# Performance work log

Measured on AMD Instinct MI355X. Metric: run time of the kernel, lower is better.

The kernel has to match this reference:

```python
import jax, jax.numpy as jnp
import numpy as np

NUM_HEADS = 16
WINDOW = 256  # window_size; tokens attend iff |i-j| <= WINDOW//2
LN_EPS = 1e-5


def setup_inputs() -> dict:
    key = jax.random.key(0)
    k1, k2, k3 = jax.random.split(key, 3)
    B, L, D = 2, 2048, 1024
    x = jax.random.normal(k1, (B, L, D), dtype=jnp.float32)
    w_qkv = jax.random.normal(k2, (3 * D, D), dtype=jnp.float32) * 0.02
    w_out = jax.random.normal(k3, (D, D), dtype=jnp.float32) * 0.02
    gamma = jnp.ones((D,), dtype=jnp.float32)
    beta = jnp.zeros((D,), dtype=jnp.float32)
    return {"x": x, "w_qkv": w_qkv, "w_out": w_out, "gamma": gamma, "beta": beta}


def reference(x, w_qkv, w_out, gamma, beta):
    B, L, D = x.shape
    H = NUM_HEADS
    HD = D // H
    residual = x
    # LayerNorm
    mu = jnp.mean(x, axis=-1, keepdims=True)
    var = jnp.mean(jnp.square(x - mu), axis=-1, keepdims=True)
    xn = (x - mu) * jax.lax.rsqrt(var + LN_EPS) * gamma + beta
    # QKV projection (torch Linear: y = x @ W.T)
    qkv = jnp.einsum('bld,ed->ble', xn, w_qkv).reshape(B, L, 3, H, HD)
    qkv = jnp.transpose(qkv, (2, 0, 3, 1, 4))  # [3, B, H, L, HD]
    q, k, v = qkv[0], qkv[1], qkv[2]
    # Dense scores with banded window mask (same math as the torch module)
    scores = jnp.einsum('bhqd,bhkd->bhqk', q, k) / jnp.sqrt(jnp.float32(HD))
    idx = jnp.arange(L)
    band = jnp.abs(idx[:, None] - idx[None, :]) <= (WINDOW // 2)  # [L, L] bool
    scores = jnp.where(band[None, None], scores, -jnp.inf)
    attn = jax.nn.softmax(scores, axis=-1)
    out = jnp.einsum('bhqk,bhkd->bhqd', attn, v)  # [B, H, L, HD]
    out = jnp.transpose(out, (0, 2, 1, 3)).reshape(B, L, D)
    return residual + jnp.einsum('bld,ed->ble', out, w_out)
```

## Files before the change

kernel.cpp:

```cpp
#include <hip/hip_runtime.h>

typedef unsigned int u32;
typedef unsigned short u16;
typedef __attribute__((ext_vector_type(8))) short short8;
typedef __attribute__((ext_vector_type(4))) float f32x4;

#define LSEQ 2048
#define DM 1024
#define HWIN 128
#define QSCALE 0.1803368801111204f

__device__ __forceinline__ u32 pk(float lo, float hi) {
  u32 r;
  asm("v_cvt_pk_bf16_f32 %0, %1, %2" : "=v"(r) : "v"(lo), "v"(hi));
  return r;
}
__device__ __forceinline__ u16 f2bf(float f) {
  union { float f; u32 u; } v; v.f = f;
  u32 r = v.u + 0x7FFFu + ((v.u >> 16) & 1u);
  return (u16)(r >> 16);
}
__device__ __forceinline__ u32 packbf(float lo, float hi) {
  return (u32)f2bf(lo) | ((u32)f2bf(hi) << 16);
}

typedef __attribute__((address_space(3))) u32 lds_u32;
typedef __attribute__((address_space(1))) const u32 glob_u32;
__device__ __forceinline__ void g2lds16(const void* g, void* l) {
  __builtin_amdgcn_global_load_lds((glob_u32*)g, (lds_u32*)l, 16, 0, 0);
}

__global__ __launch_bounds__(256) void ln_cvt_kernel(const float* __restrict__ x,
                                                     const float* __restrict__ gamma,
                                                     const float* __restrict__ beta,
                                                     u16* __restrict__ xn,
                                                     const float* __restrict__ wqi,
                                                     const float* __restrict__ woi,
                                                     u16* __restrict__ wq,
                                                     u16* __restrict__ wo) {
  int blk = blockIdx.x;
  int t = threadIdx.x;
  if (blk >= 4096) {
    const float* in; u16* out; int i;
    if (blk < 7168) { in = wqi; out = wq; i = (blk - 4096) * 256 + t; }
    else            { in = woi; out = wo; i = (blk - 7168) * 256 + t; }
    float4 v = ((const float4*)in)[i];
    u32* dst = (u32*)out + i * 2;
    dst[0] = pk(v.x, v.y);
    dst[1] = pk(v.z, v.w);
    return;
  }
  int r = blk;
  const float4* xr = (const float4*)(x + (size_t)r * DM);
  float4 v = xr[t];
  float s = v.x + v.y + v.z + v.w;
  float s2 = v.x * v.x + v.y * v.y + v.z * v.z + v.w * v.w;
#pragma unroll
  for (int o = 32; o; o >>= 1) { s += __shfl_xor(s, o); s2 += __shfl_xor(s2, o); }
  __shared__ float ws1[4], ws2[4];
  if ((t & 63) == 0) { ws1[t >> 6] = s; ws2[t >> 6] = s2; }
  __syncthreads();
  s = ws1[0] + ws1[1] + ws1[2] + ws1[3];
  s2 = ws2[0] + ws2[1] + ws2[2] + ws2[3];
  float mu = s * (1.0f / DM);
  float var = s2 * (1.0f / DM) - mu * mu;
  float rs = rsqrtf(var + 1e-5f);
  float4 g = ((const float4*)gamma)[t];
  float4 b = ((const float4*)beta)[t];
  u32* dst = (u32*)(xn + (size_t)r * DM) + t * 2;
  dst[0] = pk((v.x - mu) * rs * g.x + b.x, (v.y - mu) * rs * g.y + b.y);
  dst[1] = pk((v.z - mu) * rs * g.z + b.z, (v.w - mu) * rs * g.w + b.w);
}

__device__ __forceinline__ void stage_tile(const u16* __restrict__ G, int gr0, int K,
                                           int k0, u16* lbuf, int tid, int w) {
#pragma unroll
  for (int j = 0; j < 4; ++j) {
    int rp = j * 32 + (tid >> 3);
    int ce = ((tid & 7) ^ (rp & 7)) * 8;
    g2lds16(G + (size_t)(gr0 + rp) * K + k0 + ce, lbuf + j * 2048 + w * 512);
  }
}

template <int MODE>
__global__ __launch_bounds__(256) void gemm_bt(const u16* __restrict__ Ag,
                                               const u16* __restrict__ Bg,
                                               int K, int NB, int NT,
                                               u16* __restrict__ qk_out,
                                               u16* __restrict__ vt_out,
                                               const float* __restrict__ resid,
                                               float* __restrict__ out) {
  __shared__ __align__(16) u16 sm[32768];
  int tid = threadIdx.x;
  int w = tid >> 6, l = tid & 63;
  int lg = l >> 4, li = l & 15;
  int wr = w >> 1, wc = w & 1;

  for (int tile = blockIdx.x; tile < NT; tile += gridDim.x) {
    int bm = tile / NB, bn = tile % NB;
    f32x4 acc[4][4];
#pragma unroll
    for (int m = 0; m < 4; ++m)
#pragma unroll
      for (int n = 0; n < 4; ++n) acc[m][n] = (f32x4){0.f, 0.f, 0.f, 0.f};

    int nt = K >> 6;
    stage_tile(Ag, bm * 128, K, 0, sm, tid, w);
    stage_tile(Bg, bn * 128, K, 0, sm + 8192, tid, w);
    asm volatile("s_waitcnt vmcnt(0)" ::: "memory");
    __builtin_amdgcn_s_barrier();
    asm volatile("" ::: "memory");

    int cur = 0;
    for (int t = 0; t < nt; ++t) {
      if (t + 1 < nt) {
        stage_tile(Ag, bm * 128, K, (t + 1) << 6, sm + (cur ^ 1) * 16384, tid, w);
        stage_tile(Bg, bn * 128, K, (t + 1) << 6, sm + (cur ^ 1) * 16384 + 8192, tid, w);
      }
      const u16* Ab = sm + cur * 16384;
      const u16* Bb = Ab + 8192;
#pragma unroll
      for (int ks = 0; ks < 2; ++ks) {
        short8 af[4], bf4[4];
#pragma unroll
        for (int m = 0; m < 4; ++m)
          af[m] = *(const short8*)&Ab[(wr * 64 + m * 16 + li) * 64 + (((lg + ks * 4) ^ (li & 7)) * 8)];
#pragma unroll
        for (int n = 0; n < 4; ++n)
          bf4[n] = *(const short8*)&Bb[(wc * 64 + n * 16 + li) * 64 + (((lg + ks * 4) ^ (li & 7)) * 8)];
#pragma unroll
        for (int m = 0; m < 4; ++m)
#pragma unroll
          for (int n = 0; n < 4; ++n)
            acc[m][n] = __builtin_amdgcn_mfma_f32_16x16x32_bf16(af[m], bf4[n], acc[m][n], 0, 0, 0);
      }
      asm volatile("s_waitcnt vmcnt(0)" ::: "memory");
      __builtin_amdgcn_s_barrier();
      asm volatile("" ::: "memory");
      cur ^= 1;
    }

    int colbase = bn * 128 + wc * 64;
    int rowbase = bm * 128 + wr * 64;
#pragma unroll
    for (int m = 0; m < 4; ++m) {
      int row = rowbase + m * 16 + lg * 4;
#pragma unroll
      for (int n = 0; n < 4; ++n) {
        int col = colbase + n * 16 + li;
        if (MODE == 0) {
          if (colbase < 2048) {
            float qs = (colbase < 1024) ? QSCALE : 1.0f;
            u32 p01 = pk(acc[m][n][0] * qs, acc[m][n][1] * qs);
            u32 p23 = pk(acc[m][n][2] * qs, acc[m][n][3] * qs);
            qk_out[(size_t)(row + 0) * 2048 + col] = (u16)p01;
            qk_out[(size_t)(row + 1) * 2048 + col] = (u16)(p01 >> 16);
            qk_out[(size_t)(row + 2) * 2048 + col] = (u16)p23;
            qk_out[(size_t)(row + 3) * 2048 + col] = (u16)(p23 >> 16);
          } else {
            int b = row >> 11;
            int hdcol = col - 2048;
            size_t idx = ((size_t)b * 1024 + hdcol) * 2048 + (row & 2047);
            u32* d = (u32*)&vt_out[idx];
            d[0] = pk(acc[m][n][0], acc[m][n][1]);
            d[1] = pk(acc[m][n][2], acc[m][n][3]);
          }
        } else {
#pragma unroll
          for (int r = 0; r < 4; ++r) {
            size_t idx = (size_t)(row + r) * 1024 + col;
            out[idx] = resid[idx] + acc[m][n][r];
          }
        }
      }
    }
  }
}

__global__ __launch_bounds__(256) void attn_kernel(const u16* __restrict__ qk,
                                                   const u16* __restrict__ vt,
                                                   u16* __restrict__ ato) {
  __shared__ __align__(16) u16 Ks[2][2048];
  __shared__ __align__(16) u16 Vs[2][64 * 40];
  int blk0 = blockIdx.x;
  int xcd = blk0 & 7;
  int jj = blk0 >> 3;
  int bh = xcd * 4 + (jj & 3);
  int qblk = jj >> 2;
  int b = bh >> 4, h = bh & 15;
  int tid = threadIdx.x;
  int w = tid >> 6, l = tid & 63;
  int lg = l >> 4, li = l & 15;
  int qw0 = qblk * 64;
  int qw = qw0 + w * 16;
  int q = qw + li;
  int sg0 = (((2 * lg) & 3) << 4) + li;
  int sg1 = (((2 * lg + 1) & 3) << 4) + li;

  const u16* qbase = qk + (size_t)(b * 2048 + q) * 2048 + h * 64 + lg * 8;
  short8 qf0 = *(const short8*)qbase;
  short8 qf1 = *(const short8*)(qbase + 32);

  f32x4 o0 = {0,0,0,0}, o1 = {0,0,0,0}, o2 = {0,0,0,0}, o3 = {0,0,0,0};
  float lsum = 0.f;

  int blo = qw0 - HWIN; if (blo < 0) blo = 0;
  int bhi = qw0 + 63 + HWIN; if (bhi > LSEQ - 1) bhi = LSEQ - 1;
  int kb0 = blo & ~31;
  int nc = ((bhi - kb0) >> 5) + 1;
  int wlo = qw - HWIN, whi = qw + 15 + HWIN;

  int krow = tid >> 3, kcl = tid & 7;
  const u16* ksrc0 = qk + (size_t)b * 2048 * 2048 + 1024 + h * 64 + ((kcl ^ (krow & 7)) * 8);
  u16* kdst = &Ks[0][0] + (size_t)tid * 8;
  int vrow = tid >> 2, vc = tid & 3;
  const u16* vsrc0 = vt + (size_t)(bh * 64 + vrow) * 2048 + vc * 8;

  g2lds16(ksrc0 + (size_t)(kb0 + krow) * 2048, kdst);
  short8 vreg = *(const short8*)(vsrc0 + kb0);
  *(short8*)(&Vs[0][0] + vrow * 40 + vc * 8) = vreg;
  __syncthreads();

  int cur = 0;
  for (int c = 0; c < nc; ++c) {
    int kb = kb0 + (c << 5);
    if (c + 1 < nc) {
      g2lds16(ksrc0 + (size_t)(kb + 32 + krow) * 2048, kdst + (cur ^ 1) * 2048);
      vreg = *(const short8*)(vsrc0 + kb + 32);
    }

    if (kb + 31 >= wlo && kb <= whi) {
      const u16* Kb = &Ks[cur][0];
      const u16* Vb = &Vs[cur][0];
      int p1 = ((lg ^ (li & 7)) * 8);
      int p2 = p1 ^ 32;
      short8 k00 = *(const short8*)&Kb[li * 64 + p1];
      short8 k01 = *(const short8*)&Kb[li * 64 + p2];
      short8 k10 = *(const short8*)&Kb[(li + 16) * 64 + p1];
      short8 k11 = *(const short8*)&Kb[(li + 16) * 64 + p2];
      f32x4 c0 = {0,0,0,0}, c1 = {0,0,0,0};
      c0 = __builtin_amdgcn_mfma_f32_16x16x32_bf16(k00, qf0, c0, 0, 0, 0);
      c0 = __builtin_amdgcn_mfma_f32_16x16x32_bf16(k01, qf1, c0, 0, 0, 0);
      c1 = __builtin_amdgcn_mfma_f32_16x16x32_bf16(k10, qf0, c1, 0, 0, 0);
      c1 = __builtin_amdgcn_mfma_f32_16x16x32_bf16(k11, qf1, c1, 0, 0, 0);

      float p[8];
      bool interior = (kb >= qw + 15 - HWIN) && (kb + 31 <= qw + HWIN);
      if (interior) {
#pragma unroll
        for (int r = 0; r < 4; ++r) {
          p[r]     = __builtin_amdgcn_exp2f(c0[r]);
          p[r + 4] = __builtin_amdgcn_exp2f(c1[r]);
        }
      } else {
        int kd = kb + lg * 4 - q;
#pragma unroll
        for (int r = 0; r < 4; ++r) {
          int d0 = kd + r, d1 = d0 + 16;
          p[r]     = (d0 >= -HWIN && d0 <= HWIN) ? __builtin_amdgcn_exp2f(c0[r]) : 0.f;
          p[r + 4] = (d1 >= -HWIN && d1 <= HWIN) ? __builtin_amdgcn_exp2f(c1[r]) : 0.f;
        }
      }
      lsum += ((p[0] + p[1]) + (p[2] + p[3])) + ((p[4] + p[5]) + (p[6] + p[7]));

      u32 a0 = packbf(p[0], p[1]);
      u32 a1 = packbf(p[2], p[3]);
      u32 b0 = packbf(p[4], p[5]);
      u32 b1 = packbf(p[6], p[7]);
      u32 w0 = (u32)__shfl((int)a0, sg0), w1 = (u32)__shfl((int)a1, sg0);
      u32 w2 = (u32)__shfl((int)a0, sg1), w3 = (u32)__shfl((int)a1, sg1);
      u32 x0 = (u32)__shfl((int)b0, sg0), x1 = (u32)__shfl((int)b1, sg0);
      u32 x2 = (u32)__shfl((int)b0, sg1), x3 = (u32)__shfl((int)b1, sg1);
      bool lohalf = lg < 2;
      union { u32 u[4]; short8 s; } pf;
      pf.u[0] = lohalf ? w0 : x0;
      pf.u[1] = lohalf ? w1 : x1;
      pf.u[2] = lohalf ? w2 : x2;
      pf.u[3] = lohalf ? w3 : x3;

      short8 v0 = *(const short8*)&Vb[(li     ) * 40 + lg * 8];
      short8 v1 = *(const short8*)&Vb[(li + 16) * 40 + lg * 8];
      short8 v2 = *(const short8*)&Vb[(li + 32) * 40 + lg * 8];
      short8 v3 = *(const short8*)&Vb[(li + 48) * 40 + lg * 8];
      o0 = __builtin_amdgcn_mfma_f32_16x16x32_bf16(v0, pf.s, o0, 0, 0, 0);
      o1 = __builtin_amdgcn_mfma_f32_16x16x32_bf16(v1, pf.s, o1, 0, 0, 0);
      o2 = __builtin_amdgcn_mfma_f32_16x16x32_bf16(v2, pf.s, o2, 0, 0, 0);
      o3 = __builtin_amdgcn_mfma_f32_16x16x32_bf16(v3, pf.s, o3, 0, 0, 0);
    }

    if (c + 1 < nc) {
      *(short8*)(&Vs[cur ^ 1][0] + vrow * 40 + vc * 8) = vreg;
    }
    __syncthreads();
    cur ^= 1;
  }

  lsum += __shfl_xor(lsum, 16);
  lsum += __shfl_xor(lsum, 32);
  float inv = 1.0f / lsum;
  u16* orow = ato + (size_t)(b * 2048 + q) * 1024 + h * 64 + lg * 4;
  *(u32*)(orow +  0) = pk(o0[0] * inv, o0[1] * inv);
  *(u32*)(orow +  2) = pk(o0[2] * inv, o0[3] * inv);
  *(u32*)(orow + 16) = pk(o1[0] * inv, o1[1] * inv);
  *(u32*)(orow + 18) = pk(o1[2] * inv, o1[3] * inv);
  *(u32*)(orow + 32) = pk(o2[0] * inv, o2[1] * inv);
  *(u32*)(orow + 34) = pk(o2[2] * inv, o2[3] * inv);
  *(u32*)(orow + 48) = pk(o3[0] * inv, o3[1] * inv);
  *(u32*)(orow + 50) = pk(o3[2] * inv, o3[3] * inv);
}

extern "C" void kernel_launch(void* const* d_in, const int* in_sizes, int n_in,
                              void* d_out, int out_size, void* d_ws, size_t ws_size,
                              hipStream_t stream) {
  const float* x     = (const float*)d_in[0];
  const float* w_qkv = (const float*)d_in[1];
  const float* w_out = (const float*)d_in[2];
  const float* gamma = (const float*)d_in[3];
  const float* beta  = (const float*)d_in[4];
  float* out = (float*)d_out;
  char* ws = (char*)d_ws;

  u16* xn  = (u16*)(ws);
  u16* wq  = (u16*)(ws + 8388608);
  u16* wo  = (u16*)(ws + 14680064);
  u16* qkb = (u16*)(ws + 16777216);
  u16* vt  = (u16*)(ws + 33554432);
  u16* ao  = (u16*)(ws + 41943040);

  ln_cvt_kernel<<<8192, 256, 0, stream>>>(x, gamma, beta, xn, w_qkv, w_out, wq, wo);
  gemm_bt<0><<<512, 256, 0, stream>>>(xn, wq, 1024, 24, 768, qkb, vt, nullptr, nullptr);
  attn_kernel<<<1024, 256, 0, stream>>>(qkb, vt, ao);
  gemm_bt<1><<<256, 256, 0, stream>>>(ao, wo, 1024, 8, 256, nullptr, nullptr, x, out);
}
```

Before: 87.20 us.

## Widen attention blocks to 128 queries with 64-key double-buffered chunks

The attention kernel now runs 8 waves per block over 128 queries instead of 4 waves over 64. Each iteration stages 64 keys and values into shared memory and processes them as two 32-key sub-steps. This spreads each K/V halo load across more queries and halves the number of barrier-separated iterations per key range. In exchange it uses more shared memory per block and launches half as many blocks, which may lower occupancy. The QKV GEMM launch grid is also raised from 512 to 768 blocks.

```diff
diff --git a/kernel.cpp b/kernel.cpp
--- a/kernel.cpp
+++ b/kernel.cpp
@@ -177,11 +177,11 @@
   }
 }
 
-__global__ __launch_bounds__(256) void attn_kernel(const u16* __restrict__ qk,
+__global__ __launch_bounds__(512) void attn_kernel(const u16* __restrict__ qk,
                                                    const u16* __restrict__ vt,
                                                    u16* __restrict__ ato) {
-  __shared__ __align__(16) u16 Ks[2][2048];
-  __shared__ __align__(16) u16 Vs[2][64 * 40];
+  __shared__ __align__(16) u16 Ks[2][4096];
+  __shared__ __align__(16) u16 Vs[2][64 * 72];
   int blk0 = blockIdx.x;
   int xcd = blk0 & 7;
   int jj = blk0 >> 3;
@@ -191,7 +191,7 @@
   int tid = threadIdx.x;
   int w = tid >> 6, l = tid & 63;
   int lg = l >> 4, li = l & 15;
-  int qw0 = qblk * 64;
+  int qw0 = qblk * 128;
   int qw = qw0 + w * 16;
   int q = qw + li;
   int sg0 = (((2 * lg) & 3) << 4) + li;
@@ -205,91 +205,97 @@
   float lsum = 0.f;
 
   int blo = qw0 - HWIN; if (blo < 0) blo = 0;
-  int bhi = qw0 + 63 + HWIN; if (bhi > LSEQ - 1) bhi = LSEQ - 1;
-  int kb0 = blo & ~31;
-  int nc = ((bhi - kb0) >> 5) + 1;
+  int bhi = qw0 + 127 + HWIN; if (bhi > LSEQ - 1) bhi = LSEQ - 1;
+  int kb0 = blo & ~63;
+  int nph = ((bhi - kb0) >> 6) + 1;
   int wlo = qw - HWIN, whi = qw + 15 + HWIN;
 
   int krow = tid >> 3, kcl = tid & 7;
   const u16* ksrc0 = qk + (size_t)b * 2048 * 2048 + 1024 + h * 64 + ((kcl ^ (krow & 7)) * 8);
   u16* kdst = &Ks[0][0] + (size_t)tid * 8;
-  int vrow = tid >> 2, vc = tid & 3;
+  int vrow = tid >> 3, vc = tid & 7;
   const u16* vsrc0 = vt + (size_t)(bh * 64 + vrow) * 2048 + vc * 8;
 
   g2lds16(ksrc0 + (size_t)(kb0 + krow) * 2048, kdst);
   short8 vreg = *(const short8*)(vsrc0 + kb0);
-  *(short8*)(&Vs[0][0] + vrow * 40 + vc * 8) = vreg;
+  *(short8*)(&Vs[0][0] + vrow * 72 + vc * 8) = vreg;
   __syncthreads();
 
   int cur = 0;
-  for (int c = 0; c < nc; ++c) {
-    int kb = kb0 + (c << 5);
-    if (c + 1 < nc) {
-      g2lds16(ksrc0 + (size_t)(kb + 32 + krow) * 2048, kdst + (cur ^ 1) * 2048);
-      vreg = *(const short8*)(vsrc0 + kb + 32);
-    }
-
-    if (kb + 31 >= wlo && kb <= whi) {
-      const u16* Kb = &Ks[cur][0];
-      const u16* Vb = &Vs[cur][0];
-      int p1 = ((lg ^ (li & 7)) * 8);
-      int p2 = p1 ^ 32;
-      short8 k00 = *(const short8*)&Kb[li * 64 + p1];
-      short8 k01 = *(const short8*)&Kb[li * 64 + p2];
-      short8 k10 = *(const short8*)&Kb[(li + 16) * 64 + p1];
-      short8 k11 = *(const short8*)&Kb[(li + 16) * 64 + p2];
-      f32x4 c0 = {0,0,0,0}, c1 = {0,0,0,0};
-      c0 = __builtin_amdgcn_mfma_f32_16x16x32_bf16(k00, qf0, c0, 0, 0, 0);
-      c0 = __builtin_amdgcn_mfma_f32_16x16x32_bf16(k01, qf1, c0, 0, 0, 0);
-      c1 = __builtin_amdgcn_mfma_f32_16x16x32_bf16(k10, qf0, c1, 0, 0, 0);
-      c1 = __builtin_amdgcn_mfma_f32_16x16x32_bf16(k11, qf1, c1, 0, 0, 0);
-
-      float p[8];
-      bool interior = (kb >= qw + 15 - HWIN) && (kb + 31 <= qw + HWIN);
-      if (interior) {
-#pragma unroll
-        for (int r = 0; r < 4; ++r) {
-          p[r]     = __builtin_amdgcn_exp2f(c0[r]);
-          p[r + 4] = __builtin_amdgcn_exp2f(c1[r]);
+  for (int c = 0; c < nph; ++c) {
+    int kb = kb0 + (c << 6);
+    if (c + 1 < nph) {
+      g2lds16(ksrc0 + (size_t)(kb + 64 + krow) * 2048, kdst + (cur ^ 1) * 4096);
+      vreg = *(const short8*)(vsrc0 + kb + 64);
+    }
+    const u16* Kb = &Ks[cur][0];
+    const u16* Vb = &Vs[cur][0];
+    int p1 = ((lg ^ (li & 7)) * 8);
+    int p2 = p1 ^ 32;
+
+#pragma unroll
+    for (int sub = 0; sub < 2; ++sub) {
+      int kbs = kb + sub * 32;
+      if (kbs + 31 >= wlo && kbs <= whi) {
+        const u16* kr0 = &Kb[(sub * 32 + li) * 64];
+        const u16* kr1 = &Kb[(sub * 32 + li + 16) * 64];
+        short8 k00 = *(const short8*)(kr0 + p1);
+        short8 k01 = *(const short8*)(kr0 + p2);
+        short8 k10 = *(const short8*)(kr1 + p1);
+        short8 k11 = *(const short8*)(kr1 + p2);
+        f32x4 c0 = {0,0,0,0}, c1 = {0,0,0,0};
+        c0 = __builtin_amdgcn_mfma_f32_16x16x32_bf16(k00, qf0, c0, 0, 0, 0);
+        c0 = __builtin_amdgcn_mfma_f32_16x16x32_bf16(k01, qf1, c0, 0, 0, 0);
+        c1 = __builtin_amdgcn_mfma_f32_16x16x32_bf16(k10, qf0, c1, 0, 0, 0);
+        c1 = __builtin_amdgcn_mfma_f32_16x16x32_bf16(k11, qf1, c1, 0, 0, 0);
+
+        float p[8];
+        bool interior = (kbs >= qw + 15 - HWIN) && (kbs + 31 <= qw + HWIN);
+        if (interior) {
+#pragma unroll
+          for (int r = 0; r < 4; ++r) {
+            p[r]     = __builtin_amdgcn_exp2f(c0[r]);
+            p[r + 4] = __builtin_amdgcn_exp2f(c1[r]);
+          }
+        } else {
+          int kd = kbs + lg * 4 - q;
+#pragma unroll
+          for (int r = 0; r < 4; ++r) {
+            int d0 = kd + r, d1 = d0 + 16;
+            p[r]     = (d0 >= -HWIN && d0 <= HWIN) ? __builtin_amdgcn_exp2f(c0[r]) : 0.f;
+            p[r + 4] = (d1 >= -HWIN && d1 <= HWIN) ? __builtin_amdgcn_exp2f(c1[r]) : 0.f;
+          }
         }
-      } else {
-        int kd = kb + lg * 4 - q;
-#pragma unroll
-        for (int r = 0; r < 4; ++r) {
-          int d0 = kd + r, d1 = d0 + 16;
-          p[r]     = (d0 >= -HWIN && d0 <= HWIN) ? __builtin_amdgcn_exp2f(c0[r]) : 0.f;
-          p[r + 4] = (d1 >= -HWIN && d1 <= HWIN) ? __builtin_amdgcn_exp2f(c1[r]) : 0.f;
-        }
+        lsum += ((p[0] + p[1]) + (p[2] + p[3])) + ((p[4] + p[5]) + (p[6] + p[7]));
+
+        u32 a0 = packbf(p[0], p[1]);
+        u32 a1 = packbf(p[2], p[3]);
+        u32 b0 = packbf(p[4], p[5]);
+        u32 b1 = packbf(p[6], p[7]);
+        u32 w0 = (u32)__shfl((int)a0, sg0), w1 = (u32)__shfl((int)a1, sg0);
+        u32 w2 = (u32)__shfl((int)a0, sg1), w3 = (u32)__shfl((int)a1, sg1);
+        u32 x0 = (u32)__shfl((int)b0, sg0), x1 = (u32)__shfl((int)b1, sg0);
+        u32 x2 = (u32)__shfl((int)b0, sg1), x3 = (u32)__shfl((int)b1, sg1);
+        bool lohalf = lg < 2;
+        union { u32 u[4]; short8 s; } pf;
+        pf.u[0] = lohalf ? w0 : x0;
+        pf.u[1] = lohalf ? w1 : x1;
+        pf.u[2] = lohalf ? w2 : x2;
+        pf.u[3] = lohalf ? w3 : x3;
+
+        short8 v0 = *(const short8*)&Vb[(li     ) * 72 + sub * 32 + lg * 8];
+        short8 v1 = *(const short8*)&Vb[(li + 16) * 72 + sub * 32 + lg * 8];
+        short8 v2 = *(const short8*)&Vb[(li + 32) * 72 + sub * 32 + lg * 8];
+        short8 v3 = *(const short8*)&Vb[(li + 48) * 72 + sub * 32 + lg * 8];
+        o0 = __builtin_amdgcn_mfma_f32_16x16x32_bf16(v0, pf.s, o0, 0, 0, 0);
+        o1 = __builtin_amdgcn_mfma_f32_16x16x32_bf16(v1, pf.s, o1, 0, 0, 0);
+        o2 = __builtin_amdgcn_mfma_f32_16x16x32_bf16(v2, pf.s, o2, 0, 0, 0);
+        o3 = __builtin_amdgcn_mfma_f32_16x16x32_bf16(v3, pf.s, o3, 0, 0, 0);
       }
-      lsum += ((p[0] + p[1]) + (p[2] + p[3])) + ((p[4] + p[5]) + (p[6] + p[7]));
-
-      u32 a0 = packbf(p[0], p[1]);
-      u32 a1 = packbf(p[2], p[3]);
-      u32 b0 = packbf(p[4], p[5]);
-      u32 b1 = packbf(p[6], p[7]);
-      u32 w0 = (u32)__shfl((int)a0, sg0), w1 = (u32)__shfl((int)a1, sg0);
-      u32 w2 = (u32)__shfl((int)a0, sg1), w3 = (u32)__shfl((int)a1, sg1);
-      u32 x0 = (u32)__shfl((int)b0, sg0), x1 = (u32)__shfl((int)b1, sg0);
-      u32 x2 = (u32)__shfl((int)b0, sg1), x3 = (u32)__shfl((int)b1, sg1);
-      bool lohalf = lg < 2;
-      union { u32 u[4]; short8 s; } pf;
-      pf.u[0] = lohalf ? w0 : x0;
-      pf.u[1] = lohalf ? w1 : x1;
-      pf.u[2] = lohalf ? w2 : x2;
-      pf.u[3] = lohalf ? w3 : x3;
-
-      short8 v0 = *(const short8*)&Vb[(li     ) * 40 + lg * 8];
-      short8 v1 = *(const short8*)&Vb[(li + 16) * 40 + lg * 8];
-      short8 v2 = *(const short8*)&Vb[(li + 32) * 40 + lg * 8];
-      short8 v3 = *(const short8*)&Vb[(li + 48) * 40 + lg * 8];
-      o0 = __builtin_amdgcn_mfma_f32_16x16x32_bf16(v0, pf.s, o0, 0, 0, 0);
-      o1 = __builtin_amdgcn_mfma_f32_16x16x32_bf16(v1, pf.s, o1, 0, 0, 0);
-      o2 = __builtin_amdgcn_mfma_f32_16x16x32_bf16(v2, pf.s, o2, 0, 0, 0);
-      o3 = __builtin_amdgcn_mfma_f32_16x16x32_bf16(v3, pf.s, o3, 0, 0, 0);
-    }
-
-    if (c + 1 < nc) {
-      *(short8*)(&Vs[cur ^ 1][0] + vrow * 40 + vc * 8) = vreg;
+    }
+
+    if (c + 1 < nph) {
+      *(short8*)(&Vs[cur ^ 1][0] + vrow * 72 + vc * 8) = vreg;
     }
     __syncthreads();
     cur ^= 1;
@@ -328,7 +334,7 @@
   u16* ao  = (u16*)(ws + 41943040);
 
   ln_cvt_kernel<<<8192, 256, 0, stream>>>(x, gamma, beta, xn, w_qkv, w_out, wq, wo);
-  gemm_bt<0><<<512, 256, 0, stream>>>(xn, wq, 1024, 24, 768, qkb, vt, nullptr, nullptr);
-  attn_kernel<<<1024, 256, 0, stream>>>(qkb, vt, ao);
+  gemm_bt<0><<<768, 256, 0, stream>>>(xn, wq, 1024, 24, 768, qkb, vt, nullptr, nullptr);
+  attn_kernel<<<512, 512, 0, stream>>>(qkb, vt, ao);
   gemm_bt<1><<<256, 256, 0, stream>>>(ao, wo, 1024, 8, 256, nullptr, nullptr, x, out);
 }
```

Result: slower. 92.25 us (+5.8%).

## Use triple-buffered K=32 LDS pipeline in GEMM and launch one block per tile

Applied to the files above, without the earlier changes.

Replaces the double-buffered K=64 tile staging with a three-stage ring of K=32 slices. Loads for step t+2 are issued while step t computes, and the wait uses a partial vmcnt so the next stage's loads can stay in flight. LDS per block drops from 64KB to 48KB, which may let more blocks fit per CU. The QKV GEMM grid also grows from 512 to 768 so each block handles one tile instead of looping. The cost is twice as many barriers per K pass and a new XOR swizzle for the narrower rows.

```diff
diff --git a/kernel.cpp b/kernel.cpp
--- a/kernel.cpp
+++ b/kernel.cpp
@@ -72,13 +72,13 @@
   dst[1] = pk((v.z - mu) * rs * g.z + b.z, (v.w - mu) * rs * g.w + b.w);
 }
 
-__device__ __forceinline__ void stage_tile(const u16* __restrict__ G, int gr0, int K,
-                                           int k0, u16* lbuf, int tid, int w) {
-#pragma unroll
-  for (int j = 0; j < 4; ++j) {
-    int rp = j * 32 + (tid >> 3);
-    int ce = ((tid & 7) ^ (rp & 7)) * 8;
-    g2lds16(G + (size_t)(gr0 + rp) * K + k0 + ce, lbuf + j * 2048 + w * 512);
+__device__ __forceinline__ void stage32(const u16* __restrict__ G, int gr0, int K,
+                                        int k0, u16* lbuf, int tid, int w) {
+#pragma unroll
+  for (int j = 0; j < 2; ++j) {
+    int rp = j * 64 + (tid >> 2);
+    int sc = ((tid & 3) ^ ((tid >> 3) & 3)) * 8;
+    g2lds16(G + (size_t)(gr0 + rp) * K + k0 + sc, lbuf + j * 2048 + w * 512);
   }
 }
 
@@ -90,7 +90,7 @@
                                                u16* __restrict__ vt_out,
                                                const float* __restrict__ resid,
                                                float* __restrict__ out) {
-  __shared__ __align__(16) u16 sm[32768];
+  __shared__ __align__(16) u16 sm[24576];
   int tid = threadIdx.x;
   int w = tid >> 6, l = tid & 63;
   int lg = l >> 4, li = l & 15;
@@ -104,40 +104,44 @@
 #pragma unroll
       for (int n = 0; n < 4; ++n) acc[m][n] = (f32x4){0.f, 0.f, 0.f, 0.f};
 
-    int nt = K >> 6;
-    stage_tile(Ag, bm * 128, K, 0, sm, tid, w);
-    stage_tile(Bg, bn * 128, K, 0, sm + 8192, tid, w);
-    asm volatile("s_waitcnt vmcnt(0)" ::: "memory");
+    int nt = K >> 5;
+    stage32(Ag, bm * 128, K, 0, sm, tid, w);
+    stage32(Bg, bn * 128, K, 0, sm + 4096, tid, w);
+    stage32(Ag, bm * 128, K, 32, sm + 8192, tid, w);
+    stage32(Bg, bn * 128, K, 32, sm + 12288, tid, w);
+    asm volatile("s_waitcnt vmcnt(4)" ::: "memory");
     __builtin_amdgcn_s_barrier();
     asm volatile("" ::: "memory");
 
     int cur = 0;
+    int sl = (li >> 1) & 3;
     for (int t = 0; t < nt; ++t) {
-      if (t + 1 < nt) {
-        stage_tile(Ag, bm * 128, K, (t + 1) << 6, sm + (cur ^ 1) * 16384, tid, w);
-        stage_tile(Bg, bn * 128, K, (t + 1) << 6, sm + (cur ^ 1) * 16384 + 8192, tid, w);
+      if (t + 2 < nt) {
+        int nb = cur + 2; if (nb >= 3) nb -= 3;
+        stage32(Ag, bm * 128, K, (t + 2) << 5, sm + nb * 8192, tid, w);
+        stage32(Bg, bn * 128, K, (t + 2) << 5, sm + nb * 8192 + 4096, tid, w);
       }
-      const u16* Ab = sm + cur * 16384;
-      const u16* Bb = Ab + 8192;
-#pragma unroll
-      for (int ks = 0; ks < 2; ++ks) {
-        short8 af[4], bf4[4];
-#pragma unroll
-        for (int m = 0; m < 4; ++m)
-          af[m] = *(const short8*)&Ab[(wr * 64 + m * 16 + li) * 64 + (((lg + ks * 4) ^ (li & 7)) * 8)];
+      const u16* Ab = sm + cur * 8192;
+      const u16* Bb = Ab + 4096;
+      short8 af[4], bf4[4];
+#pragma unroll
+      for (int m = 0; m < 4; ++m)
+        af[m] = *(const short8*)&Ab[(wr * 64 + m * 16 + li) * 32 + ((lg ^ sl) * 8)];
+#pragma unroll
+      for (int n = 0; n < 4; ++n)
+        bf4[n] = *(const short8*)&Bb[(wc * 64 + n * 16 + li) * 32 + ((lg ^ sl) * 8)];
+#pragma unroll
+      for (int m = 0; m < 4; ++m)
 #pragma unroll
         for (int n = 0; n < 4; ++n)
-          bf4[n] = *(const short8*)&Bb[(wc * 64 + n * 16 + li) * 64 + (((lg + ks * 4) ^ (li & 7)) * 8)];
-#pragma unroll
-        for (int m = 0; m < 4; ++m)
-#pragma unroll
-          for (int n = 0; n < 4; ++n)
-            acc[m][n] = __builtin_amdgcn_mfma_f32_16x16x32_bf16(af[m], bf4[n], acc[m][n], 0, 0, 0);
-      }
-      asm volatile("s_waitcnt vmcnt(0)" ::: "memory");
+          acc[m][n] = __builtin_amdgcn_mfma_f32_16x16x32_bf16(af[m], bf4[n], acc[m][n], 0, 0, 0);
+      if (t + 2 < nt)
+        asm volatile("s_waitcnt vmcnt(4)" ::: "memory");
+      else
+        asm volatile("s_waitcnt vmcnt(0)" ::: "memory");
       __builtin_amdgcn_s_barrier();
       asm volatile("" ::: "memory");
-      cur ^= 1;
+      cur = (cur == 2) ? 0 : cur + 1;
     }
 
     int colbase = bn * 128 + wc * 64;
@@ -328,7 +332,7 @@
   u16* ao  = (u16*)(ws + 41943040);
 
   ln_cvt_kernel<<<8192, 256, 0, stream>>>(x, gamma, beta, xn, w_qkv, w_out, wq, wo);
-  gemm_bt<0><<<512, 256, 0, stream>>>(xn, wq, 1024, 24, 768, qkb, vt, nullptr, nullptr);
+  gemm_bt<0><<<768, 256, 0, stream>>>(xn, wq, 1024, 24, 768, qkb, vt, nullptr, nullptr);
   attn_kernel<<<1024, 256, 0, stream>>>(qkb, vt, ao);
   gemm_bt<1><<<256, 256, 0, stream>>>(ao, wo, 1024, 8, 256, nullptr, nullptr, x, out);
 }
```

Result: slower. 94.55 us (+8.4%).
